# Kernel optimization log

Hardware: AMD Instinct MI355X
Metric: run time of the kernel (lower is better)

The kernel has to match this reference:

```python
import jax, jax.numpy as jnp
import numpy as np

D_MODEL = 1024
N_HEADS = 16
D_FF = 4096
B = 8
S_TGT = 1024
S_SRC = 1024


def layer_norm(x, g, b, eps=1e-5):
    mu = jnp.mean(x, axis=-1, keepdims=True)
    var = jnp.mean(jnp.square(x - mu), axis=-1, keepdims=True)
    return (x - mu) * jax.lax.rsqrt(var + eps) * g + b


def mha(q_in, k_in, v_in, Wq, bq, Wk, bk, Wv, bv, Wo, bo, mask):
    Bq, Sq, D = q_in.shape
    hd = D // N_HEADS

    def split(t):
        return t.reshape(t.shape[0], t.shape[1], N_HEADS, hd).transpose(0, 2, 1, 3)

    Q = split(q_in @ Wq + bq)   # [B,H,Sq,hd]
    K = split(k_in @ Wk + bk)   # [B,H,Sk,hd]
    V = split(v_in @ Wv + bv)
    scores = jnp.einsum('bhqd,bhkd->bhqk', Q, K) / jnp.sqrt(jnp.float32(hd))
    scores = jnp.where(mask, scores, jnp.float32(-1e9))
    attn = jax.nn.softmax(scores, axis=-1)
    out = jnp.einsum('bhqk,bhkd->bhqd', attn, V)
    out = out.transpose(0, 2, 1, 3).reshape(Bq, Sq, D)
    return out @ Wo + bo


def setup_inputs() -> dict:
    key = jax.random.key(0)
    ks = jax.random.split(key, 32)
    s = 0.02
    inp = {
        'x': jax.random.normal(ks[0], (B, S_TGT, D_MODEL), dtype=jnp.float32),
        'encoder_output': jax.random.normal(ks[1], (B, S_SRC, D_MODEL), dtype=jnp.float32),
        'tgt_mask': jnp.tril(jnp.ones((S_TGT, S_TGT), dtype=bool))[None, None],
        'src_mask': jnp.ones((1, 1, S_TGT, S_SRC), dtype=bool),
    }
    i = 2
    for p in ('sa', 'ca'):
        for w in ('Wq', 'Wk', 'Wv', 'Wo'):
            inp[f'{p}_{w}'] = jax.random.normal(ks[i], (D_MODEL, D_MODEL), dtype=jnp.float32) * s
            inp[f'{p}_b{w[1].lower()}'] = jnp.zeros((D_MODEL,), dtype=jnp.float32)
            i += 1
    inp['ff_W1'] = jax.random.normal(ks[i], (D_MODEL, D_FF), dtype=jnp.float32) * s; i += 1
    inp['ff_b1'] = jnp.zeros((D_FF,), dtype=jnp.float32)
    inp['ff_W2'] = jax.random.normal(ks[i], (D_FF, D_MODEL), dtype=jnp.float32) * s; i += 1
    inp['ff_b2'] = jnp.zeros((D_MODEL,), dtype=jnp.float32)
    for n in ('ln1', 'ln2', 'ln3'):
        inp[f'{n}_g'] = jnp.ones((D_MODEL,), dtype=jnp.float32)
        inp[f'{n}_b'] = jnp.zeros((D_MODEL,), dtype=jnp.float32)
    return inp


def reference(x, encoder_output, tgt_mask, src_mask,
              sa_Wq, sa_bq, sa_Wk, sa_bk, sa_Wv, sa_bv, sa_Wo, sa_bo,
              ca_Wq, ca_bq, ca_Wk, ca_bk, ca_Wv, ca_bv, ca_Wo, ca_bo,
              ff_W1, ff_b1, ff_W2, ff_b2,
              ln1_g, ln1_b, ln2_g, ln2_b, ln3_g, ln3_b):
    # masked self-attention + residual + LN (dropout = identity in eval mode)
    attn = mha(x, x, x, sa_Wq, sa_bq, sa_Wk, sa_bk, sa_Wv, sa_bv, sa_Wo, sa_bo, tgt_mask)
    x = layer_norm(x + attn, ln1_g, ln1_b)
    # cross-attention to encoder output
    cross = mha(x, encoder_output, encoder_output,
                ca_Wq, ca_bq, ca_Wk, ca_bk, ca_Wv, ca_bv, ca_Wo, ca_bo, src_mask)
    x = layer_norm(x + cross, ln2_g, ln2_b)
    # position-wise FFN: Linear -> ReLU -> Linear
    ff = jax.nn.relu(x @ ff_W1 + ff_b1) @ ff_W2 + ff_b2
    x = layer_norm(x + ff, ln3_g, ln3_b)
    return x
```

## Files before the change

### kernel.cpp

```cpp
#include <hip/hip_runtime.h>
#include <math.h>

typedef __attribute__((ext_vector_type(8))) short short8;
typedef __attribute__((ext_vector_type(4))) short short4v;
typedef __attribute__((ext_vector_type(4))) float floatx4;
typedef __attribute__((ext_vector_type(16))) float floatx16;

__device__ inline float bf2f(unsigned short h) {
    unsigned int u = ((unsigned int)h) << 16;
    float f;
    __builtin_memcpy(&f, &u, 4);
    return f;
}
__device__ inline unsigned short f2bf(float f) {
    unsigned int u;
    __builtin_memcpy(&u, &f, 4);
    u = (u + 0x7fffu + ((u >> 16) & 1u)) >> 16;
    return (unsigned short)u;
}
__device__ inline unsigned int f2u(float f) {
    return __builtin_bit_cast(unsigned int, f);
}

__device__ inline void gld_lds16(const unsigned short* g, unsigned short* l) {
    __builtin_amdgcn_global_load_lds(
        (const __attribute__((address_space(1))) unsigned int*)g,
        (__attribute__((address_space(3))) unsigned int*)l, 16, 0, 0);
}

__global__ __launch_bounds__(256) void detect_dtype(
    const unsigned short* __restrict__ x, int* __restrict__ flag) {
    __shared__ int s[4];
    int bad = 0;
    for (int i = threadIdx.x; i < 8192; i += 256) {
        float v = bf2f(x[i]);
        if (!(fabsf(v) <= 1.0e4f)) bad = 1;
    }
    unsigned long long b = __ballot(bad);
    int wave = threadIdx.x >> 6;
    if ((threadIdx.x & 63) == 0) s[wave] = (b != 0ULL) ? 1 : 0;
    __syncthreads();
    if (threadIdx.x == 0) flag[0] = s[0] | s[1] | s[2] | s[3];
}

__global__ __launch_bounds__(256) void to_bf16_kernel(
    const void* __restrict__ in, unsigned short* __restrict__ out,
    const int* __restrict__ flag, int n8) {
    int fl = flag[0];
    int i = blockIdx.x * 256 + threadIdx.x;
    if (i >= n8) return;
    size_t off = (size_t)i * 8;
    if (fl) {
        floatx4 f0 = *(const floatx4*)((const float*)in + off);
        floatx4 f1 = *(const floatx4*)((const float*)in + off + 4);
        short8 v;
#pragma unroll
        for (int j = 0; j < 4; j++) {
            v[j] = (short)f2bf(f0[j]);
            v[4 + j] = (short)f2bf(f1[j]);
        }
        *(short8*)(out + off) = v;
    } else {
        *(short8*)(out + off) = *(const short8*)((const unsigned short*)in + off);
    }
}

__global__ __launch_bounds__(256) void transpose_any(
    const void* __restrict__ in, unsigned short* __restrict__ out,
    int rows, int cols, const int* __restrict__ flag) {
    int fl = flag ? flag[0] : 0;
    __shared__ unsigned short t[32][33];
    int tx = threadIdx.x & 31, ty = threadIdx.x >> 5;
    int c0 = blockIdx.x * 32, r0 = blockIdx.y * 32;
    size_t base = (size_t)blockIdx.z * rows * cols;
#pragma unroll
    for (int k = 0; k < 4; k++) {
        size_t idx = base + (size_t)(r0 + ty + k * 8) * cols + c0 + tx;
        t[ty + k * 8][tx] = fl ? f2bf(((const float*)in)[idx])
                               : ((const unsigned short*)in)[idx];
    }
    __syncthreads();
#pragma unroll
    for (int k = 0; k < 4; k++)
        out[base + (size_t)(c0 + ty + k * 8) * rows + r0 + tx] = t[tx][ty + k * 8];
}

struct Ptr8 { const void* p[8]; };
__global__ __launch_bounds__(256) void transpose8(
    Ptr8 in, unsigned short* __restrict__ out, const int* __restrict__ flag) {
    int fl = flag[0];
    __shared__ unsigned short t[32][33];
    const void* src = in.p[blockIdx.z];
    unsigned short* dst = out + (size_t)blockIdx.z * 1024 * 1024;
    int tx = threadIdx.x & 31, ty = threadIdx.x >> 5;
    int c0 = blockIdx.x * 32, r0 = blockIdx.y * 32;
#pragma unroll
    for (int k = 0; k < 4; k++) {
        size_t idx = (size_t)(r0 + ty + k * 8) * 1024 + c0 + tx;
        t[ty + k * 8][tx] = fl ? f2bf(((const float*)src)[idx])
                               : ((const unsigned short*)src)[idx];
    }
    __syncthreads();
#pragma unroll
    for (int k = 0; k < 4; k++)
        dst[(size_t)(c0 + ty + k * 8) * 1024 + r0 + tx] = t[tx][ty + k * 8];
}

__device__ inline void stage_half(const unsigned short* __restrict__ G, int ldk,
                                  int grow, int gcol, unsigned short* ldsb,
                                  int tid) {
    int s0 = tid, s1 = tid + 512;
    int r0 = s0 >> 3, c0 = ((s0 & 7) ^ (r0 & 7)) << 3;
    int r1 = s1 >> 3, c1 = ((s1 & 7) ^ (r1 & 7)) << 3;
    gld_lds16(&G[(size_t)(grow + r0) * ldk + gcol + c0], &ldsb[s0 * 8]);
    gld_lds16(&G[(size_t)(grow + r1) * ldk + gcol + c1], &ldsb[s1 * 8]);
}

template <int BN_, int EPI>
__global__ __launch_bounds__(512) void gemm8(
    const unsigned short* __restrict__ A, const unsigned short* __restrict__ Bt,
    const void* __restrict__ b0, const void* __restrict__ b1,
    const void* __restrict__ b2, unsigned short* __restrict__ C0,
    unsigned short* __restrict__ C1, unsigned short* __restrict__ C2,
    int M, int N, int K, const int* __restrict__ flag) {
    constexpr int NR = BN_ / 64;
    constexpr int WNT = BN_ / 4;
    constexpr int ASZ = 16384;
    constexpr int BSZ = BN_ * 64;
    __shared__ alignas(16) unsigned short lds[2 * ASZ + 2 * BSZ];

    const int tid = threadIdx.x;
    const int lane = tid & 63, wave = tid >> 6;
    const int quad = lane >> 4, l16 = lane & 15, x7 = l16 & 7;
    const int wm = wave >> 2, wn = wave & 3;
    const int bm = blockIdx.x * 256, bn = blockIdx.y * BN_;
    const int NT = K >> 6;

    floatx4 acc[8][NR];
#pragma unroll
    for (int i = 0; i < 8; ++i)
#pragma unroll
        for (int j = 0; j < NR; ++j) acc[i][j] = (floatx4){0.f, 0.f, 0.f, 0.f};

    stage_half(A, K, bm, 0, lds, tid);
    stage_half(A, K, bm + 128, 0, lds + 8192, tid);
    stage_half(Bt, K, bn, 0, lds + 2 * ASZ, tid);
    if (BN_ == 256) stage_half(Bt, K, bn + 128, 0, lds + 2 * ASZ + 8192, tid);
    asm volatile("s_waitcnt vmcnt(0)" ::: "memory");
    __builtin_amdgcn_s_barrier();

    short8 bfr[NR][2], afr[2][2][2];

    for (int it = 0; it < NT; ++it) {
        unsigned short* const Ac = lds + (it & 1) * ASZ;
        unsigned short* const Bc = lds + 2 * ASZ + (it & 1) * BSZ;
        unsigned short* const An = lds + ((it + 1) & 1) * ASZ;
        unsigned short* const Bn = lds + 2 * ASZ + ((it + 1) & 1) * BSZ;
        const bool more = (it + 1 < NT);
        if (more) {
            const int kn = (it + 1) << 6;
            stage_half(A, K, bm, kn, An, tid);
            stage_half(A, K, bm + 128, kn, An + 8192, tid);
            stage_half(Bt, K, bn, kn, Bn, tid);
            if (BN_ == 256) stage_half(Bt, K, bn + 128, kn, Bn + 8192, tid);
        }
#pragma unroll
        for (int ni = 0; ni < NR; ++ni)
#pragma unroll
            for (int ks = 0; ks < 2; ++ks)
                bfr[ni][ks] = *(const short8*)&Bc[
                    (wn * WNT + ni * 16 + l16) * 64 +
                    ((((ks << 2) + quad) ^ x7) << 3)];
#pragma unroll
        for (int m2 = 0; m2 < 2; ++m2)
#pragma unroll
            for (int ks = 0; ks < 2; ++ks)
                afr[0][m2][ks] = *(const short8*)&Ac[
                    (wm * 128 + m2 * 16 + l16) * 64 +
                    ((((ks << 2) + quad) ^ x7) << 3)];
#pragma unroll
        for (int q = 0; q < 4; ++q) {
            if (q < 3) {
#pragma unroll
                for (int m2 = 0; m2 < 2; ++m2)
#pragma unroll
                    for (int ks = 0; ks < 2; ++ks)
                        afr[(q + 1) & 1][m2][ks] = *(const short8*)&Ac[
                            (wm * 128 + ((q + 1) * 2 + m2) * 16 + l16) * 64 +
                            ((((ks << 2) + quad) ^ x7) << 3)];
            }
            __builtin_amdgcn_s_setprio(1);
#pragma unroll
            for (int m2 = 0; m2 < 2; ++m2)
#pragma unroll
                for (int ni = 0; ni < NR; ++ni) {
                    acc[q * 2 + m2][ni] = __builtin_amdgcn_mfma_f32_16x16x32_bf16(
                        bfr[ni][0], afr[q & 1][m2][0], acc[q * 2 + m2][ni], 0, 0, 0);
                    acc[q * 2 + m2][ni] = __builtin_amdgcn_mfma_f32_16x16x32_bf16(
                        bfr[ni][1], afr[q & 1][m2][1], acc[q * 2 + m2][ni], 0, 0, 0);
                }
            __builtin_amdgcn_s_setprio(0);
        }
        if (more) {
            asm volatile("s_waitcnt vmcnt(0)" ::: "memory");
            __builtin_amdgcn_s_barrier();
        }
    }

    const int fl = flag[0];
    const void* bp = b0;
    unsigned short* Cp = C0;
    int mode = 0;
    int cb = bn;
    if (EPI == 1) mode = 1;
    if (EPI == 4) mode = 2;
    if (EPI == 2) {
        int ch = bn >> 10;
        cb = bn & 1023;
        bp = (ch == 0) ? b0 : (ch == 1) ? b1 : b2;
        Cp = (ch == 0) ? C0 : (ch == 1) ? C1 : C2;
        mode = (ch == 0) ? 2 : (ch == 1) ? 3 : 4;
    }
    if (EPI == 3) {
        int ch = bn >> 10;
        cb = bn & 1023;
        bp = (ch == 0) ? b0 : b1;
        Cp = (ch == 0) ? C0 : C1;
        mode = (ch == 0) ? 3 : 4;
    }
#pragma unroll
    for (int ni = 0; ni < NR; ++ni) {
        const int colb = cb + wn * WNT + ni * 16 + quad * 4;
        float b4[4];
        if (fl) {
            floatx4 t = *(const floatx4*)&((const float*)bp)[colb];
#pragma unroll
            for (int r = 0; r < 4; ++r) b4[r] = t[r];
        } else {
            short4v t = *(const short4v*)&((const unsigned short*)bp)[colb];
#pragma unroll
            for (int r = 0; r < 4; ++r) b4[r] = bf2f((unsigned short)t[r]);
        }
        const int hh = colb >> 6, dd = colb & 63;
#pragma unroll
        for (int mi = 0; mi < 8; ++mi) {
            const int row = bm + wm * 128 + mi * 16 + l16;
            short4v pk;
#pragma unroll
            for (int r = 0; r < 4; ++r) {
                float v = acc[mi][ni][r] + b4[r];
                if (mode == 1) v = fmaxf(v, 0.f);
                if (mode == 2) v *= 0.18033688f;
                pk[r] = (short)f2bf(v);
            }
            if (mode <= 1) {
                *(short4v*)&Cp[(size_t)row * N + colb] = pk;
            } else {
                const int b_ = row >> 10, s_ = row & 1023;
                if (mode != 4) {
                    *(short4v*)&Cp[((((size_t)b_ * 16 + hh) * 1024) + s_) * 64 + dd] = pk;
                } else {
#pragma unroll
                    for (int r = 0; r < 4; ++r)
                        Cp[(((size_t)b_ * 16 + hh) * 64 + dd + r) * 1024 + s_] =
                            (unsigned short)pk[r];
                }
            }
        }
    }
}

template <int CAUSAL>
__global__ __launch_bounds__(256) void attn_kernel(
    const unsigned short* __restrict__ Q, const unsigned short* __restrict__ K,
    const unsigned short* __restrict__ Vt, unsigned short* __restrict__ O,
    int Skv) {
    __shared__ alignas(16) unsigned short Ks[2][512 * 8];
    __shared__ alignas(16) unsigned short Vs[2][512 * 8];
    const int S = 1024;
    int tid = threadIdx.x, wave = tid >> 6, lane = tid & 63;
    int h = lane >> 5, l31 = lane & 31;
    int fid = blockIdx.y * 8 + blockIdx.x;
    int bh = fid & 127;
    int qt = fid >> 7;
    if (CAUSAL) qt = 7 - qt;
    const int qb = qt * 128 + wave * 32;
    const unsigned short* Qp = Q + (size_t)bh * S * 64;
    const unsigned short* Kp = K + (size_t)bh * Skv * 64;
    const unsigned short* Vp = Vt + (size_t)bh * 64 * Skv;

    short8 qf[4];
#pragma unroll
    for (int t = 0; t < 4; t++)
        qf[t] = *(const short8*)&Qp[(qb + l31) * 64 + t * 16 + h * 8];

    floatx16 o[2];
#pragma unroll
    for (int dn = 0; dn < 2; dn++)
#pragma unroll
        for (int rr = 0; rr < 16; rr++) o[dn][rr] = 0.f;
    float m = -1e30f, l = 0.f;
    const int kend = CAUSAL ? (qt + 1) * 128 : Skv;
    const int nch = kend >> 6;

    int sr0 = tid >> 3, sc0 = (tid & 7) ^ (sr0 & 7);
    int sr1 = (tid + 256) >> 3, sc1 = ((tid + 256) & 7) ^ (sr1 & 7);

    auto stageKV = [&](int kb, int b) {
        gld_lds16(&Kp[(size_t)(kb + sr0) * 64 + sc0 * 8], &Ks[b][tid * 8]);
        gld_lds16(&Kp[(size_t)(kb + sr1) * 64 + sc1 * 8], &Ks[b][(tid + 256) * 8]);
        gld_lds16(&Vp[(size_t)sr0 * Skv + kb + sc0 * 8], &Vs[b][tid * 8]);
        gld_lds16(&Vp[(size_t)sr1 * Skv + kb + sc1 * 8], &Vs[b][(tid + 256) * 8]);
    };

    stageKV(0, 0);
    asm volatile("s_waitcnt vmcnt(0)" ::: "memory");
    __builtin_amdgcn_s_barrier();

    for (int ic = 0; ic < nch; ++ic) {
        const int kb = ic << 6, cur = ic & 1;
        const unsigned short* Ksc = Ks[cur];
        const unsigned short* Vsc = Vs[cur];
        if (ic + 1 < nch) stageKV(kb + 64, cur ^ 1);

        const bool act = !CAUSAL || (kb <= qb + 31);
        if (act) {
            floatx16 st[2];
            __builtin_amdgcn_s_setprio(1);
#pragma unroll
            for (int kg = 0; kg < 2; kg++) {
                const int row = kg * 32 + l31, r7 = row & 7;
                floatx16 z;
#pragma unroll
                for (int rr = 0; rr < 16; rr++) z[rr] = 0.f;
#pragma unroll
                for (int t = 0; t < 4; t++) {
                    short8 kf = *(const short8*)&Ksc[
                        (row * 8 + ((2 * t + h) ^ r7)) * 8];
                    z = __builtin_amdgcn_mfma_f32_32x32x16_bf16(kf, qf[t], z,
                                                                0, 0, 0);
                }
                st[kg] = z;
            }
            __builtin_amdgcn_s_setprio(0);

            if (CAUSAL && (kb + 63 > qb)) {
#pragma unroll
                for (int kg = 0; kg < 2; kg++)
#pragma unroll
                    for (int rr = 0; rr < 16; rr++) {
                        int key = kb + kg * 32 + (rr & 3) + 8 * (rr >> 2) + 4 * h;
                        if (key > qb + l31) st[kg][rr] = -1e30f;
                    }
            }
            float mx[16];
#pragma unroll
            for (int rr = 0; rr < 16; rr++) mx[rr] = fmaxf(st[0][rr], st[1][rr]);
#pragma unroll
            for (int s2 = 8; s2 > 0; s2 >>= 1)
#pragma unroll
                for (int rr = 0; rr < s2; rr++)
                    mx[rr] = fmaxf(mx[rr], mx[rr + s2]);
            float smax = fmaxf(mx[0], __shfl_xor(mx[0], 32));
            float mi = m;
            if (!__all(smax <= m + 8.f)) {
                mi = fmaxf(m, smax);
                float alpha = exp2f(m - mi);
                l *= alpha;
#pragma unroll
                for (int dn = 0; dn < 2; dn++)
#pragma unroll
                    for (int rr = 0; rr < 16; rr++) o[dn][rr] *= alpha;
                m = mi;
            }
#pragma unroll
            for (int kg = 0; kg < 2; kg++)
#pragma unroll
                for (int rr = 0; rr < 16; rr++)
                    st[kg][rr] = exp2f(st[kg][rr] - mi);
            float sm[16];
#pragma unroll
            for (int rr = 0; rr < 16; rr++) sm[rr] = st[0][rr] + st[1][rr];
#pragma unroll
            for (int s2 = 8; s2 > 0; s2 >>= 1)
#pragma unroll
                for (int rr = 0; rr < s2; rr++) sm[rr] += sm[rr + s2];
            l += sm[0] + __shfl_xor(sm[0], 32);

            unsigned int pd[2][4][2];
#pragma unroll
            for (int kg = 0; kg < 2; kg++)
#pragma unroll
                for (int g = 0; g < 4; g++)
#pragma unroll
                    for (int i = 0; i < 2; i++)
                        pd[kg][g][i] = __builtin_amdgcn_perm(
                            f2u(st[kg][4 * g + 2 * i + 1]),
                            f2u(st[kg][4 * g + 2 * i]), 0x07060302u);

            __builtin_amdgcn_s_setprio(1);
#pragma unroll
            for (int kg = 0; kg < 2; kg++)
#pragma unroll
                for (int kt = 0; kt < 2; kt++) {
                    unsigned int dw[4];
#pragma unroll
                    for (int i = 0; i < 2; i++) {
                        unsigned int a = pd[kg][2 * kt][i];
                        unsigned int b_ = pd[kg][2 * kt + 1][i];
                        unsigned int ax = (unsigned int)__shfl_xor((int)a, 32);
                        unsigned int bx = (unsigned int)__shfl_xor((int)b_, 32);
                        dw[i] = h ? bx : a;
                        dw[2 + i] = h ? b_ : ax;
                    }
                    short8 pf;
                    __builtin_memcpy(&pf, dw, 16);
#pragma unroll
                    for (int dn = 0; dn < 2; dn++) {
                        const int row = dn * 32 + l31, r7 = row & 7;
                        short8 vf = *(const short8*)&Vsc[
                            (row * 8 + ((kg * 4 + 2 * kt + h) ^ r7)) * 8];
                        o[dn] = __builtin_amdgcn_mfma_f32_32x32x16_bf16(
                            vf, pf, o[dn], 0, 0, 0);
                    }
                }
            __builtin_amdgcn_s_setprio(0);
        }

        if (ic + 1 < nch) {
            asm volatile("s_waitcnt vmcnt(0)" ::: "memory");
            __builtin_amdgcn_s_barrier();
        }
    }

    int b = bh >> 4, hh = bh & 15;
    float inv = 1.0f / l;
    size_t orow = ((size_t)(b * S + qb + l31)) * 1024 + hh * 64;
#pragma unroll
    for (int dn = 0; dn < 2; dn++)
#pragma unroll
        for (int g = 0; g < 4; g++) {
            short4v p4;
#pragma unroll
            for (int r = 0; r < 4; r++)
                p4[r] = (short)f2bf(o[dn][4 * g + r] * inv);
            *(short4v*)&O[orow + dn * 32 + 8 * g + 4 * h] = p4;
        }
}

template <int AEXT, int OEXT>
__global__ __launch_bounds__(256) void add_ln_kernel(
    const void* __restrict__ A, const unsigned short* __restrict__ Bv,
    const void* __restrict__ g, const void* __restrict__ be,
    void* __restrict__ out, const int* __restrict__ flag) {
    int fl = flag[0];
    __shared__ float red[2][4];
    int row = blockIdx.x, tid = threadIdx.x;
    size_t base = (size_t)row * 1024;
    int c = tid * 4;
    float v[4], sum = 0.f, ss = 0.f;
    if (AEXT && fl) {
        floatx4 af = *(const floatx4*)&((const float*)A)[base + c];
#pragma unroll
        for (int k = 0; k < 4; k++) v[k] = af[k];
    } else {
        short4v av = *(const short4v*)&((const unsigned short*)A)[base + c];
#pragma unroll
        for (int k = 0; k < 4; k++) v[k] = bf2f((unsigned short)av[k]);
    }
    short4v bv = *(const short4v*)&Bv[base + c];
#pragma unroll
    for (int k = 0; k < 4; k++) {
        v[k] += bf2f((unsigned short)bv[k]);
        sum += v[k];
        ss += v[k] * v[k];
    }
#pragma unroll
    for (int off = 1; off < 64; off <<= 1) {
        sum += __shfl_xor(sum, off);
        ss += __shfl_xor(ss, off);
    }
    int wave = tid >> 6, lane = tid & 63;
    if (lane == 0) {
        red[0][wave] = sum;
        red[1][wave] = ss;
    }
    __syncthreads();
    sum = red[0][0] + red[0][1] + red[0][2] + red[0][3];
    ss = red[1][0] + red[1][1] + red[1][2] + red[1][3];
    float mu = sum * (1.0f / 1024.0f);
    float var = ss * (1.0f / 1024.0f) - mu * mu;
    float rstd = rsqrtf(var + 1e-5f);
#pragma unroll
    for (int k = 0; k < 4; k++) {
        float gv = fl ? ((const float*)g)[c + k]
                      : bf2f(((const unsigned short*)g)[c + k]);
        float bev = fl ? ((const float*)be)[c + k]
                       : bf2f(((const unsigned short*)be)[c + k]);
        float y = (v[k] - mu) * rstd * gv + bev;
        if (OEXT && fl)
            ((float*)out)[base + c + k] = y;
        else
            ((unsigned short*)out)[base + c + k] = f2bf(y);
    }
}

extern "C" void kernel_launch(void* const* d_in, const int* in_sizes, int n_in,
                              void* d_out, int out_size, void* d_ws, size_t ws_size,
                              hipStream_t stream) {
    const int M = 8192;
    typedef const void* cvp;
    cvp x = d_in[0];
    cvp enc = d_in[1];
    cvp saWq = d_in[4], sabq = d_in[5];
    cvp saWk = d_in[6], sabk = d_in[7];
    cvp saWv = d_in[8], sabv = d_in[9];
    cvp saWo = d_in[10], sabo = d_in[11];
    cvp caWq = d_in[12], cabq = d_in[13];
    cvp caWk = d_in[14], cabk = d_in[15];
    cvp caWv = d_in[16], cabv = d_in[17];
    cvp caWo = d_in[18], cabo = d_in[19];
    cvp ffW1 = d_in[20], ffb1 = d_in[21];
    cvp ffW2 = d_in[22], ffb2 = d_in[23];
    cvp ln1g = d_in[24], ln1b = d_in[25];
    cvp ln2g = d_in[26], ln2b = d_in[27];
    cvp ln3g = d_in[28], ln3b = d_in[29];

    char* ws = (char*)d_ws;
    const size_t MB = 1024 * 1024;
    typedef unsigned short* up;
    up wt_sa_qkv = (up)(ws + 0);
    up wt_sa_o   = (up)(ws + 6 * MB);
    up wt_ca_q   = (up)(ws + 8 * MB);
    up wt_ca_kv  = (up)(ws + 10 * MB);
    up wt_ca_o   = (up)(ws + 14 * MB);
    up wtff1     = (up)(ws + 16 * MB);
    up wtff2     = (up)(ws + 24 * MB);
    up Qb  = (up)(ws + 32 * MB);
    up Kb  = (up)(ws + 48 * MB);
    up Vtb = (up)(ws + 64 * MB);
    up xb  = (up)(ws + 80 * MB);
    up Hb  = (up)(ws + 32 * MB);
    up Ob  = (up)(ws + 96 * MB);
    up Pb  = (up)(ws + 112 * MB);
    up x1  = (up)(ws + 128 * MB);
    up x2  = (up)(ws + 144 * MB);
    up encb = (up)(ws + 144 * MB);
    int* flag = (int*)(ws + 160 * MB);

    dim3 blk(256), blk5(512);
    detect_dtype<<<1, blk, 0, stream>>>((const unsigned short*)x, flag);

    to_bf16_kernel<<<4096, blk, 0, stream>>>(x, xb, flag, M * 1024 / 8);
    to_bf16_kernel<<<4096, blk, 0, stream>>>(enc, encb, flag, M * 1024 / 8);

    Ptr8 w8;
    w8.p[0] = saWq; w8.p[1] = saWk; w8.p[2] = saWv; w8.p[3] = saWo;
    w8.p[4] = caWq; w8.p[5] = caWk; w8.p[6] = caWv; w8.p[7] = caWo;
    transpose8<<<dim3(32, 32, 8), blk, 0, stream>>>(w8, (up)(ws + 0), flag);
    transpose_any<<<dim3(128, 32, 1), blk, 0, stream>>>(ffW1, wtff1, 1024, 4096, flag);
    transpose_any<<<dim3(32, 128, 1), blk, 0, stream>>>(ffW2, wtff2, 4096, 1024, flag);

    gemm8<256, 2><<<dim3(32, 12), blk5, 0, stream>>>(
        xb, wt_sa_qkv, sabq, sabk, sabv, Qb, Kb, Vtb, M, 3072, 1024, flag);
    attn_kernel<1><<<dim3(8, 128), blk, 0, stream>>>(Qb, Kb, Vtb, Ob, 1024);
    gemm8<128, 0><<<dim3(32, 8), blk5, 0, stream>>>(
        Ob, wt_sa_o, sabo, nullptr, nullptr, Pb, nullptr, nullptr, M, 1024, 1024, flag);
    add_ln_kernel<1, 0><<<dim3(8192), blk, 0, stream>>>(x, Pb, ln1g, ln1b, x1, flag);

    gemm8<128, 4><<<dim3(32, 8), blk5, 0, stream>>>(
        x1, wt_ca_q, cabq, nullptr, nullptr, Qb, nullptr, nullptr, M, 1024, 1024, flag);
    gemm8<256, 3><<<dim3(32, 8), blk5, 0, stream>>>(
        encb, wt_ca_kv, cabk, cabv, nullptr, Kb, Vtb, nullptr, M, 2048, 1024, flag);
    attn_kernel<0><<<dim3(8, 128), blk, 0, stream>>>(Qb, Kb, Vtb, Ob, 1024);
    gemm8<128, 0><<<dim3(32, 8), blk5, 0, stream>>>(
        Ob, wt_ca_o, cabo, nullptr, nullptr, Pb, nullptr, nullptr, M, 1024, 1024, flag);
    add_ln_kernel<0, 0><<<dim3(8192), blk, 0, stream>>>(x1, Pb, ln2g, ln2b, x2, flag);

    gemm8<256, 1><<<dim3(32, 16), blk5, 0, stream>>>(
        x2, wtff1, ffb1, nullptr, nullptr, Hb, nullptr, nullptr, M, 4096, 1024, flag);
    gemm8<128, 0><<<dim3(32, 8), blk5, 0, stream>>>(
        Hb, wtff2, ffb2, nullptr, nullptr, Pb, nullptr, nullptr, M, 1024, 4096, flag);
    add_ln_kernel<0, 1><<<dim3(8192), blk, 0, stream>>>(x2, Pb, ln3g, ln3b, d_out, flag);
}
```

Measured before the change: 775.4 us.

## Stage GEMM epilogue through swizzled LDS for 16-byte stores; use raw v_exp

The GEMM epilogue now writes bias-added bf16 tiles into a per-wave XOR-swizzled LDS region and reads them back so each lane issues 16-byte row-contiguous global stores, replacing scattered 8-byte stores. The transposed V path is kept separate and unchanged. The attention softmax now calls v_exp_f32 directly through inline asm instead of exp2f, which drops the range and denormal handling around it. The staging adds a barrier and LDS traffic and reuses the GEMM's shared buffer, which must be large enough for 128*WNT elements per wave.

After: 703.4 us. 1.1x faster.

```diff
diff --git a/kernel.cpp b/kernel.cpp
--- a/kernel.cpp
+++ b/kernel.cpp
@@ -20,6 +20,11 @@
 }
 __device__ inline unsigned int f2u(float f) {
     return __builtin_bit_cast(unsigned int, f);
+}
+__device__ inline float exp2_raw(float x) {
+    float r;
+    asm("v_exp_f32 %0, %1" : "=v"(r) : "v"(x));
+    return r;
 }
 
 __device__ inline void gld_lds16(const unsigned short* g, unsigned short* l) {
@@ -228,43 +233,83 @@
         Cp = (ch == 0) ? C0 : C1;
         mode = (ch == 0) ? 3 : 4;
     }
-#pragma unroll
-    for (int ni = 0; ni < NR; ++ni) {
-        const int colb = cb + wn * WNT + ni * 16 + quad * 4;
-        float b4[4];
-        if (fl) {
-            floatx4 t = *(const floatx4*)&((const float*)bp)[colb];
-#pragma unroll
-            for (int r = 0; r < 4; ++r) b4[r] = t[r];
-        } else {
-            short4v t = *(const short4v*)&((const unsigned short*)bp)[colb];
-#pragma unroll
-            for (int r = 0; r < 4; ++r) b4[r] = bf2f((unsigned short)t[r]);
-        }
-        const int hh = colb >> 6, dd = colb & 63;
-#pragma unroll
-        for (int mi = 0; mi < 8; ++mi) {
-            const int row = bm + wm * 128 + mi * 16 + l16;
-            short4v pk;
-#pragma unroll
-            for (int r = 0; r < 4; ++r) {
-                float v = acc[mi][ni][r] + b4[r];
-                if (mode == 1) v = fmaxf(v, 0.f);
-                if (mode == 2) v *= 0.18033688f;
-                pk[r] = (short)f2bf(v);
-            }
+
+    if (mode == 4) {
+#pragma unroll
+        for (int ni = 0; ni < NR; ++ni) {
+            const int colb = cb + wn * WNT + ni * 16 + quad * 4;
+            float b4[4];
+            if (fl) {
+                floatx4 t = *(const floatx4*)&((const float*)bp)[colb];
+#pragma unroll
+                for (int r = 0; r < 4; ++r) b4[r] = t[r];
+            } else {
+                short4v t = *(const short4v*)&((const unsigned short*)bp)[colb];
+#pragma unroll
+                for (int r = 0; r < 4; ++r) b4[r] = bf2f((unsigned short)t[r]);
+            }
+            const int hh = colb >> 6, dd = colb & 63;
+#pragma unroll
+            for (int mi = 0; mi < 8; ++mi) {
+                const int row = bm + wm * 128 + mi * 16 + l16;
+                const int b_ = row >> 10, s_ = row & 1023;
+#pragma unroll
+                for (int r = 0; r < 4; ++r) {
+                    float v = acc[mi][ni][r] + b4[r];
+                    Cp[(((size_t)b_ * 16 + hh) * 64 + dd + r) * 1024 + s_] = f2bf(v);
+                }
+            }
+        }
+    } else {
+        constexpr int SLOTS = WNT / 8;
+        constexpr int SMASK = SLOTS - 1;
+        __syncthreads();
+        unsigned short* W2 = lds + wave * (128 * WNT);
+#pragma unroll
+        for (int ni = 0; ni < NR; ++ni) {
+            const int colb = cb + wn * WNT + ni * 16 + quad * 4;
+            float b4[4];
+            if (fl) {
+                floatx4 t = *(const floatx4*)&((const float*)bp)[colb];
+#pragma unroll
+                for (int r = 0; r < 4; ++r) b4[r] = t[r];
+            } else {
+                short4v t = *(const short4v*)&((const unsigned short*)bp)[colb];
+#pragma unroll
+                for (int r = 0; r < 4; ++r) b4[r] = bf2f((unsigned short)t[r]);
+            }
+            const int cslot = ni * 2 + (quad >> 1);
+            const int chalf = quad & 1;
+#pragma unroll
+            for (int mi = 0; mi < 8; ++mi) {
+                const int r = mi * 16 + l16;
+                short4v pk;
+#pragma unroll
+                for (int rr = 0; rr < 4; ++rr) {
+                    float v = acc[mi][ni][rr] + b4[rr];
+                    if (mode == 1) v = fmaxf(v, 0.f);
+                    if (mode == 2) v *= 0.18033688f;
+                    pk[rr] = (short)f2bf(v);
+                }
+                *(short4v*)&W2[r * WNT + ((cslot ^ (r & SMASK)) << 3) +
+                               (chalf << 2)] = pk;
+            }
+        }
+        const int lslot = lane & SMASK;
+        const int lrow = lane / SLOTS;
+        constexpr int RPP = 64 / SLOTS;
+#pragma unroll
+        for (int p = 0; p < 128 / RPP; ++p) {
+            const int r = p * RPP + lrow;
+            short8 v = *(const short8*)&W2[r * WNT + ((lslot ^ (r & SMASK)) << 3)];
+            const int colg = cb + wn * WNT + (lslot << 3);
+            const int rowg = bm + wm * 128 + r;
             if (mode <= 1) {
-                *(short4v*)&Cp[(size_t)row * N + colb] = pk;
+                *(short8*)&Cp[(size_t)rowg * N + colg] = v;
             } else {
-                const int b_ = row >> 10, s_ = row & 1023;
-                if (mode != 4) {
-                    *(short4v*)&Cp[((((size_t)b_ * 16 + hh) * 1024) + s_) * 64 + dd] = pk;
-                } else {
-#pragma unroll
-                    for (int r = 0; r < 4; ++r)
-                        Cp[(((size_t)b_ * 16 + hh) * 64 + dd + r) * 1024 + s_] =
-                            (unsigned short)pk[r];
-                }
+                const int b_ = rowg >> 10, s_ = rowg & 1023;
+                const int hh2 = colg >> 6, dd2 = colg & 63;
+                *(short8*)&Cp[((((size_t)b_ * 16 + hh2) * 1024) + s_) * 64 + dd2] = v;
             }
         }
     }
@@ -365,7 +410,7 @@
             float mi = m;
             if (!__all(smax <= m + 8.f)) {
                 mi = fmaxf(m, smax);
-                float alpha = exp2f(m - mi);
+                float alpha = exp2_raw(m - mi);
                 l *= alpha;
 #pragma unroll
                 for (int dn = 0; dn < 2; dn++)
@@ -377,7 +422,7 @@
             for (int kg = 0; kg < 2; kg++)
 #pragma unroll
                 for (int rr = 0; rr < 16; rr++)
-                    st[kg][rr] = exp2f(st[kg][rr] - mi);
+                    st[kg][rr] = exp2_raw(st[kg][rr] - mi);
             float sm[16];
 #pragma unroll
             for (int rr = 0; rr < 16; rr++) sm[rr] = st[0][rr] + st[1][rr];
```
